# Kernel tuning notes

Measured on AMD Instinct MI355X. Metric: run time of the kernel, lower is better.

Reference implementation:

```python
import jax, jax.numpy as jnp
import numpy as np


def avg_pool2(x):
    # 2x2 average pool, stride 2, NCHW
    b, c, h, w = x.shape
    return x.reshape(b, c, h // 2, 2, w // 2, 2).mean(axis=(3, 5))


def bisr_conv(x, W, mvk, mvb, beta):
    # ReDistribution: per-channel affine
    x = x * mvk + mvb
    # Spectral binary activation with tanh STE (forward value == sign(x))
    t = jnp.tanh(x * beta)
    xb = jax.lax.stop_gradient(jnp.sign(x)) - jax.lax.stop_gradient(t) + t
    # Binary weights: per-output-channel scale * sign(W), clipped-weight STE
    scale = jnp.mean(jnp.abs(W), axis=(1, 2, 3), keepdims=True)  # [O,1,1,1]
    bw_ng = jax.lax.stop_gradient(scale * jnp.sign(W))
    cw = jnp.clip(W, -1.0, 1.0)
    bw = bw_ng - jax.lax.stop_gradient(cw) + cw
    return jax.lax.conv_general_dilated(
        xb, bw, window_strides=(1, 1), padding=((1, 1), (1, 1)),
        dimension_numbers=('NCHW', 'OIHW', 'NCHW'))


def rprelu(x, pb0, alpha, pb1):
    x = x + pb0
    x = jnp.where(x >= 0, x, alpha * x)  # per-channel PReLU
    return x + pb1


def setup_inputs() -> dict:
    key = jax.random.key(0)
    B, C, H, W = 16, 128, 128, 128
    ks = jax.random.split(key, 3)
    x = jax.random.normal(ks[0], (B, C, H, W), dtype=jnp.float32)
    def branch_params(k):
        Wt = jax.random.normal(k, (C, C, 3, 3), dtype=jnp.float32) * 0.001
        return Wt
    zeros_c = jnp.zeros((1, C, 1, 1), jnp.float32)
    ones_c = jnp.ones((1, C, 1, 1), jnp.float32)
    alpha = jnp.full((1, C, 1, 1), 0.25, jnp.float32)
    return {
        'x': x,
        'W1': branch_params(ks[1]), 'mvk1': ones_c, 'mvb1': zeros_c,
        'beta1': jnp.ones((1,), jnp.float32), 'pb0_1': zeros_c,
        'alpha1': alpha, 'pb1_1': zeros_c,
        'W2': branch_params(ks[2]), 'mvk2': ones_c, 'mvb2': zeros_c,
        'beta2': jnp.ones((1,), jnp.float32), 'pb0_2': zeros_c,
        'alpha2': alpha, 'pb1_2': zeros_c,
    }


def reference(x, W1, mvk1, mvb1, beta1, pb0_1, alpha1, pb1_1,
              W2, mvk2, mvb2, beta2, pb0_2, alpha2, pb1_2):
    out = avg_pool2(x)  # [B, C, H/2, W/2]
    out1 = out + rprelu(bisr_conv(out, W1, mvk1, mvb1, beta1), pb0_1, alpha1, pb1_1)
    out2 = out + rprelu(bisr_conv(out, W2, mvk2, mvb2, beta2), pb0_2, alpha2, pb1_2)
    return jnp.concatenate([out1, out2], axis=1)  # [B, 2C, H/2, W/2]
```

## Files before the change

### kernel.cpp

```cpp
#include <hip/hip_runtime.h>
#include <stdint.h>

#define BATCH 16
#define CH    128
#define HIN   128
#define WIN   128
#define PH    64
#define PW    64

#define OFF_ABITS  33554432u
#define OFF_WBITS  35651584u
#define OFF_WSCALE 35688448u

__global__ __launch_bounds__(256) void pool_pack(
    const float* __restrict__ x,
    const float* __restrict__ mvk1, const float* __restrict__ mvb1,
    const float* __restrict__ mvk2, const float* __restrict__ mvb2,
    float* __restrict__ pooled, uint32_t* __restrict__ abits)
{
    __shared__ float sp[CH][PW + 1];
    const int b  = blockIdx.y;
    const int ph = blockIdx.x;
    const int t  = threadIdx.x;
    const int pw = t & 63;
    const int c0 = t >> 6;

    for (int cg = 0; cg < CH; cg += 4) {
        const int c = cg + c0;
        const float* xrow = x + (((size_t)(b * CH + c) * HIN) + 2 * ph) * WIN;
        const float2 r0 = *(const float2*)(xrow + 2 * pw);
        const float2 r1 = *(const float2*)(xrow + WIN + 2 * pw);
        const float pv = (r0.x + r0.y + r1.x + r1.y) * 0.25f;
        pooled[(size_t)(b * CH + c) * (PH * PW) + ph * PW + pw] = pv;
        sp[c][pw] = pv;
    }
    __syncthreads();

    const int branch = c0 >> 1;
    const int wp0    = (c0 & 1) * 2;
    const float* mvk = branch ? mvk2 : mvk1;
    const float* mvb = branch ? mvb2 : mvb1;
    for (int wi = 0; wi < 2; ++wi) {
        const int word = wp0 + wi;
        uint32_t bits = 0;
        #pragma unroll
        for (int j = 0; j < 32; ++j) {
            const int c = word * 32 + j;
            const float v = sp[c][pw] * mvk[c] + mvb[c];
            bits |= (v < 0.0f ? 1u : 0u) << j;
        }
        abits[((size_t)(branch * BATCH + b) * (PH * PW) + ph * PW + pw) * 4 + word] = bits;
    }
}

__global__ __launch_bounds__(64) void wprep(
    const float* __restrict__ W1, const float* __restrict__ W2,
    uint32_t* __restrict__ wbits, float* __restrict__ wscale)
{
    const int bo = blockIdx.x;
    const int branch = bo >> 7;
    const int o = bo & 127;
    const float* Wt = (branch ? W2 : W1) + (size_t)o * (CH * 9);
    const int t = threadIdx.x;

    float s = 0.f;
    for (int i = t; i < CH * 9; i += 64) s += fabsf(Wt[i]);
    #pragma unroll
    for (int off = 32; off >= 1; off >>= 1) s += __shfl_down(s, off);
    if (t == 0) wscale[bo] = s * (1.0f / (CH * 9));

    if (t < 36) {
        const int tap  = t >> 2;
        const int word = t & 3;
        uint32_t bits = 0;
        for (int j = 0; j < 32; ++j) {
            const int c = word * 32 + j;
            const float wv = Wt[c * 9 + tap];
            bits |= (wv < 0.0f ? 1u : 0u) << j;
        }
        wbits[(bo * 9 + tap) * 4 + word] = bits;
    }
}

__device__ __forceinline__ int popc4(uint4 a, uint4 w) {
    return __popc(a.x ^ w.x) + __popc(a.y ^ w.y) + __popc(a.z ^ w.z) + __popc(a.w ^ w.w);
}

__global__ __launch_bounds__(256) void bconv_main(
    const uint32_t* __restrict__ abits_, const uint32_t* __restrict__ wbits_,
    const float* __restrict__ wscale, const float* __restrict__ pooled,
    const float* __restrict__ pb0_1, const float* __restrict__ alpha1, const float* __restrict__ pb1_1,
    const float* __restrict__ pb0_2, const float* __restrict__ alpha2, const float* __restrict__ pb1_2,
    float* __restrict__ out)
{
    __shared__ uint4 ha[10][66];
    const int bid    = blockIdx.x;
    const int oh     = bid & 1;
    const int ty     = (bid >> 1) & 7;
    const int b      = (bid >> 4) & 15;
    const int branch = bid >> 8;
    const int t  = threadIdx.x;
    const int lc = t & 63;
    const int lr2 = t >> 6;

    const uint4* ab = (const uint4*)abits_ + (size_t)(branch * BATCH + b) * (PH * PW);
    for (int e = t; e < 660; e += 256) {
        const int r = e / 66, cc = e % 66;
        const int hp = ty * 8 - 1 + r;
        const int wp = cc - 1;
        uint4 v = make_uint4(0u, 0u, 0u, 0u);
        if (hp >= 0 && hp < PH && wp >= 0 && wp < PW) v = ab[hp * PW + wp];
        ha[r][cc] = v;
    }
    __syncthreads();

    uint4 a[4][3];
    #pragma unroll
    for (int rr = 0; rr < 4; ++rr)
        #pragma unroll
        for (int cc = 0; cc < 3; ++cc)
            a[rr][cc] = ha[lr2 * 2 + rr][lc + cc];

    const int gr0 = ty * 8 + lr2 * 2;
    const bool cL = (lc > 0), cR = (lc < 63);
    const bool u0 = (gr0 > 0),     d0 = (gr0 < 63);
    const bool u1 = (gr0 + 1 > 0), d1 = (gr0 + 1 < 63);

    const uint4* wb = (const uint4*)wbits_ + (size_t)branch * 128 * 9;
    const float* ws  = wscale + branch * 128;
    const float* pb0 = branch ? pb0_2  : pb0_1;
    const float* alp = branch ? alpha2 : alpha1;
    const float* pb1 = branch ? pb1_2  : pb1_1;

    const int o_beg = oh * 64, o_end = o_beg + 64;
    for (int o = o_beg; o < o_end; ++o) {
        uint4 w[9];
        #pragma unroll
        for (int tt = 0; tt < 9; ++tt) w[tt] = wb[o * 9 + tt];

        int sum0 = 0, sum1 = 0;
        #pragma unroll
        for (int dy = 0; dy < 3; ++dy) {
            #pragma unroll
            for (int dx = 0; dx < 3; ++dx) {
                const uint4 wv = w[dy * 3 + dx];
                const int p0 = popc4(a[dy][dx],     wv);
                const int p1 = popc4(a[dy + 1][dx], wv);
                const bool col_ok = (dx == 0) ? cL : ((dx == 2) ? cR : true);
                const bool r0_ok  = (dy == 0) ? u0 : ((dy == 2) ? d0 : true);
                const bool r1_ok  = (dy == 0) ? u1 : ((dy == 2) ? d1 : true);
                sum0 += (r0_ok && col_ok) ? (128 - 2 * p0) : 0;
                sum1 += (r1_ok && col_ok) ? (128 - 2 * p1) : 0;
            }
        }

        const float sc   = ws[o];
        const float b0v  = pb0[o], av = alp[o], b1v = pb1[o];
        float y0 = sc * (float)sum0 + b0v;
        float y1 = sc * (float)sum1 + b0v;
        y0 = (y0 >= 0.f) ? y0 : y0 * av;
        y1 = (y1 >= 0.f) ? y1 : y1 * av;
        y0 += b1v;
        y1 += b1v;
        const size_t pbase = (size_t)(b * CH + o) * (PH * PW) + gr0 * PW + lc;
        const float r0 = pooled[pbase]      + y0;
        const float r1 = pooled[pbase + PW] + y1;
        const size_t obase = (size_t)(b * 2 * CH + branch * CH + o) * (PH * PW) + gr0 * PW + lc;
        out[obase]      = r0;
        out[obase + PW] = r1;
    }
}

extern "C" void kernel_launch(void* const* d_in, const int* in_sizes, int n_in,
                              void* d_out, int out_size, void* d_ws, size_t ws_size,
                              hipStream_t stream)
{
    const float* x      = (const float*)d_in[0];
    const float* W1     = (const float*)d_in[1];
    const float* mvk1   = (const float*)d_in[2];
    const float* mvb1   = (const float*)d_in[3];
    const float* pb0_1  = (const float*)d_in[5];
    const float* alpha1 = (const float*)d_in[6];
    const float* pb1_1  = (const float*)d_in[7];
    const float* W2     = (const float*)d_in[8];
    const float* mvk2   = (const float*)d_in[9];
    const float* mvb2   = (const float*)d_in[10];
    const float* pb0_2  = (const float*)d_in[12];
    const float* alpha2 = (const float*)d_in[13];
    const float* pb1_2  = (const float*)d_in[14];
    float* out = (float*)d_out;

    char* ws = (char*)d_ws;
    float*    pooled = (float*)ws;
    uint32_t* abits  = (uint32_t*)(ws + OFF_ABITS);
    uint32_t* wbits  = (uint32_t*)(ws + OFF_WBITS);
    float*    wscale = (float*)(ws + OFF_WSCALE);

    hipLaunchKernelGGL(pool_pack, dim3(64, 16), dim3(256), 0, stream,
                       x, mvk1, mvb1, mvk2, mvb2, pooled, abits);
    hipLaunchKernelGGL(wprep, dim3(256), dim3(64), 0, stream, W1, W2, wbits, wscale);
    hipLaunchKernelGGL(bconv_main, dim3(512), dim3(256), 0, stream,
                       abits, wbits, wscale, pooled,
                       pb0_1, alpha1, pb1_1, pb0_2, alpha2, pb1_2, out);
}
```

Before: 323.9 us.

## Store pooled in fp16, threshold-based packing, and retile binary conv over more blocks

Pooled activations are stored as fp16 in the workspace and read back as half2 for the residual add, halving that intermediate's traffic. Activation packing now precomputes per-channel thresholds plus sign-flip masks and compares float4s from a transposed shared buffer. The conv kernel is retiled so each thread handles two adjacent columns and each block handles 16 output channels, across 2048 blocks. It also replaces boolean masking with bitmasks and closed-form base counts. The fp16 residual loses precision relative to the fp32 reference, and threshold division may differ from the affine form at exact boundaries.

```diff
diff --git a/kernel.cpp b/kernel.cpp
--- a/kernel.cpp
+++ b/kernel.cpp
@@ -8,48 +8,88 @@
 #define PH    64
 #define PW    64
 
-#define OFF_ABITS  33554432u
-#define OFF_WBITS  35651584u
-#define OFF_WSCALE 35688448u
+#define OFF_ABITS  16777216u
+#define OFF_WBITS  18874368u
+#define OFF_WSCALE 18911232u
+
+typedef _Float16 half2v __attribute__((ext_vector_type(2)));
 
 __global__ __launch_bounds__(256) void pool_pack(
     const float* __restrict__ x,
     const float* __restrict__ mvk1, const float* __restrict__ mvb1,
     const float* __restrict__ mvk2, const float* __restrict__ mvb2,
-    float* __restrict__ pooled, uint32_t* __restrict__ abits)
-{
-    __shared__ float sp[CH][PW + 1];
+    _Float16* __restrict__ pooled, uint32_t* __restrict__ abits)
+{
+    __shared__ float spT[64][132];
+    __shared__ float thrL[2][128];
+    __shared__ uint32_t flipL[2][4];
     const int b  = blockIdx.y;
     const int ph = blockIdx.x;
     const int t  = threadIdx.x;
-    const int pw = t & 63;
-    const int c0 = t >> 6;
-
-    for (int cg = 0; cg < CH; cg += 4) {
-        const int c = cg + c0;
-        const float* xrow = x + (((size_t)(b * CH + c) * HIN) + 2 * ph) * WIN;
-        const float2 r0 = *(const float2*)(xrow + 2 * pw);
-        const float2 r1 = *(const float2*)(xrow + WIN + 2 * pw);
-        const float pv = (r0.x + r0.y + r1.x + r1.y) * 0.25f;
-        pooled[(size_t)(b * CH + c) * (PH * PW) + ph * PW + pw] = pv;
-        sp[c][pw] = pv;
+
+    {
+        const int k31 = t & 31;
+        const int c0  = (t >> 5) * 16;
+        const int pw2 = k31 * 2;
+        const float* xq = x + (((size_t)b * CH) * HIN + 2 * ph) * WIN + 4 * k31;
+        for (int cg = 0; cg < 16; cg += 4) {
+            float q0[4], q1[4];
+            #pragma unroll
+            for (int u = 0; u < 4; ++u) {
+                const int c = c0 + cg + u;
+                const float* xr = xq + (size_t)c * (HIN * WIN);
+                const float4 r0 = *(const float4*)xr;
+                const float4 r1 = *(const float4*)(xr + WIN);
+                q0[u] = (r0.x + r0.y + r1.x + r1.y) * 0.25f;
+                q1[u] = (r0.z + r0.w + r1.z + r1.w) * 0.25f;
+                union { _Float16 h[2]; uint32_t w; } pk;
+                pk.h[0] = (_Float16)q0[u];
+                pk.h[1] = (_Float16)q1[u];
+                *(uint32_t*)(pooled + ((size_t)(b * CH + c) * (PH * PW)) + ph * PW + pw2) = pk.w;
+            }
+            *(float4*)&spT[pw2][c0 + cg]     = make_float4(q0[0], q0[1], q0[2], q0[3]);
+            *(float4*)&spT[pw2 + 1][c0 + cg] = make_float4(q1[0], q1[1], q1[2], q1[3]);
+        }
+    }
+
+    {
+        const int br = t >> 7, c = t & 127;
+        const float kv = (br ? mvk2 : mvk1)[c];
+        const float bv = (br ? mvb2 : mvb1)[c];
+        float thr;
+        if (kv != 0.0f) thr = -bv / kv;
+        else thr = (bv < 0.0f) ? __builtin_inff() : -__builtin_inff();
+        thrL[br][c] = thr;
+        const unsigned long long bal = __ballot(kv < 0.0f);
+        const int lane = t & 63;
+        if (lane == 0)  flipL[br][c >> 5] = (uint32_t)bal;
+        if (lane == 32) flipL[br][c >> 5] = (uint32_t)(bal >> 32);
     }
     __syncthreads();
 
-    const int branch = c0 >> 1;
-    const int wp0    = (c0 & 1) * 2;
-    const float* mvk = branch ? mvk2 : mvk1;
-    const float* mvb = branch ? mvb2 : mvb1;
-    for (int wi = 0; wi < 2; ++wi) {
-        const int word = wp0 + wi;
-        uint32_t bits = 0;
+    {
+        const int wp = t & 1;
+        const int pw = (t >> 1) & 63;
+        const int br = t >> 7;
+        const float4* prow = (const float4*)&spT[pw][wp * 64];
+        const float4* trow = (const float4*)&thrL[br][wp * 64];
+        uint32_t bits0 = 0, bits1 = 0;
         #pragma unroll
-        for (int j = 0; j < 32; ++j) {
-            const int c = word * 32 + j;
-            const float v = sp[c][pw] * mvk[c] + mvb[c];
-            bits |= (v < 0.0f ? 1u : 0u) << j;
-        }
-        abits[((size_t)(branch * BATCH + b) * (PH * PW) + ph * PW + pw) * 4 + word] = bits;
+        for (int j4 = 0; j4 < 16; ++j4) {
+            const float4 p  = prow[j4];
+            const float4 tv = trow[j4];
+            const uint32_t m = (uint32_t)(p.x < tv.x)
+                             | ((uint32_t)(p.y < tv.y) << 1)
+                             | ((uint32_t)(p.z < tv.z) << 2)
+                             | ((uint32_t)(p.w < tv.w) << 3);
+            if (j4 < 8) bits0 |= m << (j4 * 4);
+            else        bits1 |= m << ((j4 - 8) * 4);
+        }
+        bits0 ^= flipL[br][wp * 2];
+        bits1 ^= flipL[br][wp * 2 + 1];
+        uint2* ab2 = (uint2*)abits;
+        ab2[((size_t)(br * BATCH + b) * (PH * PW) + ph * PW + pw) * 2 + wp] =
+            make_uint2(bits0, bits1);
     }
 }
 
@@ -86,88 +126,84 @@
     return __popc(a.x ^ w.x) + __popc(a.y ^ w.y) + __popc(a.z ^ w.z) + __popc(a.w ^ w.w);
 }
 
-__global__ __launch_bounds__(256) void bconv_main(
+__global__ __launch_bounds__(256, 8) void bconv_main(
     const uint32_t* __restrict__ abits_, const uint32_t* __restrict__ wbits_,
-    const float* __restrict__ wscale, const float* __restrict__ pooled,
+    const float* __restrict__ wscale, const _Float16* __restrict__ pooledH,
     const float* __restrict__ pb0_1, const float* __restrict__ alpha1, const float* __restrict__ pb1_1,
     const float* __restrict__ pb0_2, const float* __restrict__ alpha2, const float* __restrict__ pb1_2,
     float* __restrict__ out)
 {
     __shared__ uint4 ha[10][66];
-    const int bid    = blockIdx.x;
-    const int oh     = bid & 1;
-    const int ty     = (bid >> 1) & 7;
-    const int b      = (bid >> 4) & 15;
-    const int branch = bid >> 8;
+    const int bid = blockIdx.x;
+    const int og     = bid & 7;
+    const int ty     = (bid >> 3) & 7;
+    const int b      = (bid >> 6) & 15;
+    const int branch = bid >> 10;
     const int t  = threadIdx.x;
-    const int lc = t & 63;
-    const int lr2 = t >> 6;
+    const int cp = t & 31;
+    const int r  = t >> 5;
+    const int gr = ty * 8 + r;
 
     const uint4* ab = (const uint4*)abits_ + (size_t)(branch * BATCH + b) * (PH * PW);
     for (int e = t; e < 660; e += 256) {
-        const int r = e / 66, cc = e % 66;
-        const int hp = ty * 8 - 1 + r;
-        const int wp = cc - 1;
+        const int rr = e / 66, cc = e % 66;
+        const int hp = ty * 8 - 1 + rr, wp = cc - 1;
         uint4 v = make_uint4(0u, 0u, 0u, 0u);
         if (hp >= 0 && hp < PH && wp >= 0 && wp < PW) v = ab[hp * PW + wp];
-        ha[r][cc] = v;
+        ha[rr][cc] = v;
     }
     __syncthreads();
 
-    uint4 a[4][3];
+    uint4 a[3][4];
     #pragma unroll
-    for (int rr = 0; rr < 4; ++rr)
+    for (int i = 0; i < 3; ++i)
         #pragma unroll
-        for (int cc = 0; cc < 3; ++cc)
-            a[rr][cc] = ha[lr2 * 2 + rr][lc + cc];
-
-    const int gr0 = ty * 8 + lr2 * 2;
-    const bool cL = (lc > 0), cR = (lc < 63);
-    const bool u0 = (gr0 > 0),     d0 = (gr0 < 63);
-    const bool u1 = (gr0 + 1 > 0), d1 = (gr0 + 1 < 63);
-
-    const uint4* wb = (const uint4*)wbits_ + (size_t)branch * 128 * 9;
-    const float* ws  = wscale + branch * 128;
+        for (int j = 0; j < 4; ++j)
+            a[i][j] = ha[r + i][2 * cp + j];
+
+    const int mr0 = (gr > 0)  ? -1 : 0;
+    const int mr2 = (gr < 63) ? -1 : 0;
+    const int mcl = (cp > 0)  ? -1 : 0;
+    const int mcr = (cp < 31) ? -1 : 0;
+    const int rowsv = 1 + (gr > 0) + (gr < 63);
+    const int base0 = 128 * rowsv * (2 + (cp > 0));
+    const int base1 = 128 * rowsv * (2 + (cp < 31));
+
+    const uint4* wb  = (const uint4*)wbits_ + (size_t)branch * (128 * 9);
+    const float* wsv = wscale + branch * 128;
     const float* pb0 = branch ? pb0_2  : pb0_1;
     const float* alp = branch ? alpha2 : alpha1;
     const float* pb1 = branch ? pb1_2  : pb1_1;
 
-    const int o_beg = oh * 64, o_end = o_beg + 64;
-    for (int o = o_beg; o < o_end; ++o) {
-        uint4 w[9];
-        #pragma unroll
-        for (int tt = 0; tt < 9; ++tt) w[tt] = wb[o * 9 + tt];
-
-        int sum0 = 0, sum1 = 0;
+    const _Float16* prow = pooledH + (size_t)(b * CH) * (PH * PW) + gr * PW + 2 * cp;
+    float* orow = out + (size_t)(b * 2 * CH + branch * CH) * (PH * PW) + gr * PW + 2 * cp;
+
+    const int o_beg = og * 16;
+    for (int o = o_beg; o < o_beg + 16; ++o) {
+        int pc0 = 0, pc1 = 0;
         #pragma unroll
         for (int dy = 0; dy < 3; ++dy) {
-            #pragma unroll
-            for (int dx = 0; dx < 3; ++dx) {
-                const uint4 wv = w[dy * 3 + dx];
-                const int p0 = popc4(a[dy][dx],     wv);
-                const int p1 = popc4(a[dy + 1][dx], wv);
-                const bool col_ok = (dx == 0) ? cL : ((dx == 2) ? cR : true);
-                const bool r0_ok  = (dy == 0) ? u0 : ((dy == 2) ? d0 : true);
-                const bool r1_ok  = (dy == 0) ? u1 : ((dy == 2) ? d1 : true);
-                sum0 += (r0_ok && col_ok) ? (128 - 2 * p0) : 0;
-                sum1 += (r1_ok && col_ok) ? (128 - 2 * p1) : 0;
-            }
-        }
-
-        const float sc   = ws[o];
-        const float b0v  = pb0[o], av = alp[o], b1v = pb1[o];
-        float y0 = sc * (float)sum0 + b0v;
-        float y1 = sc * (float)sum1 + b0v;
-        y0 = (y0 >= 0.f) ? y0 : y0 * av;
-        y1 = (y1 >= 0.f) ? y1 : y1 * av;
-        y0 += b1v;
-        y1 += b1v;
-        const size_t pbase = (size_t)(b * CH + o) * (PH * PW) + gr0 * PW + lc;
-        const float r0 = pooled[pbase]      + y0;
-        const float r1 = pooled[pbase + PW] + y1;
-        const size_t obase = (size_t)(b * 2 * CH + branch * CH + o) * (PH * PW) + gr0 * PW + lc;
-        out[obase]      = r0;
-        out[obase + PW] = r1;
+            const int mr = (dy == 0) ? mr0 : ((dy == 2) ? mr2 : -1);
+            const uint4 w0 = wb[o * 9 + dy * 3 + 0];
+            const uint4 w1 = wb[o * 9 + dy * 3 + 1];
+            const uint4 w2 = wb[o * 9 + dy * 3 + 2];
+            pc0 += popc4(a[dy][0], w0) & (mr & mcl);
+            pc1 += popc4(a[dy][1], w0) & mr;
+            pc0 += popc4(a[dy][1], w1) & mr;
+            pc1 += popc4(a[dy][2], w1) & mr;
+            pc0 += popc4(a[dy][2], w2) & mr;
+            pc1 += popc4(a[dy][3], w2) & (mr & mcr);
+        }
+        const float sc = wsv[o], b0v = pb0[o], av = alp[o], b1v = pb1[o];
+        float y0 = sc * (float)(base0 - 2 * pc0) + b0v;
+        float y1 = sc * (float)(base1 - 2 * pc1) + b0v;
+        y0 = fmaxf(y0, 0.f) + av * fminf(y0, 0.f) + b1v;
+        y1 = fmaxf(y1, 0.f) + av * fminf(y1, 0.f) + b1v;
+        const half2v pv = *(const half2v*)(prow + (size_t)o * (PH * PW));
+        float2 st;
+        st.x = (float)pv.x + y0;
+        st.y = (float)pv.y + y1;
+        *(float2*)(orow + (size_t)o * (PH * PW)) = st;
     }
 }
 
@@ -191,7 +227,7 @@
     float* out = (float*)d_out;
 
     char* ws = (char*)d_ws;
-    float*    pooled = (float*)ws;
+    _Float16* pooled = (_Float16*)ws;
     uint32_t* abits  = (uint32_t*)(ws + OFF_ABITS);
     uint32_t* wbits  = (uint32_t*)(ws + OFF_WBITS);
     float*    wscale = (float*)(ws + OFF_WSCALE);
@@ -199,7 +235,7 @@
     hipLaunchKernelGGL(pool_pack, dim3(64, 16), dim3(256), 0, stream,
                        x, mvk1, mvb1, mvk2, mvb2, pooled, abits);
     hipLaunchKernelGGL(wprep, dim3(256), dim3(64), 0, stream, W1, W2, wbits, wscale);
-    hipLaunchKernelGGL(bconv_main, dim3(512), dim3(256), 0, stream,
+    hipLaunchKernelGGL(bconv_main, dim3(2048), dim3(256), 0, stream,
                        abits, wbits, wscale, pooled,
                        pb0_1, alpha1, pb1_1, pb0_2, alpha2, pb1_2, out);
 }
```

Result: faster. 295.8 us (-8.7%).
